# Optimization experiments

Measured on AMD Instinct MI355X. Metric: run time of the kernel, lower is better.

The kernel has to match this reference:

```python
import jax, jax.numpy as jnp
import numpy as np

EMBED = 1024
HEAD = 64
B, S = 4, 4096

def setup_inputs() -> dict:
    key = jax.random.key(0)
    k1, k2, k3, k4, k5, k6 = jax.random.split(key, 6)
    scale = 1.0 / np.sqrt(EMBED)
    return {
        "query": jax.random.normal(k1, (B, S, EMBED), dtype=jnp.float32),
        "key": jax.random.normal(k2, (B, S, EMBED), dtype=jnp.float32),
        "value": jax.random.normal(k3, (B, S, EMBED), dtype=jnp.float32),
        "wq": jax.random.normal(k4, (EMBED, HEAD), dtype=jnp.float32) * scale,
        "wk": jax.random.normal(k5, (EMBED, HEAD), dtype=jnp.float32) * scale,
        "wv": jax.random.normal(k6, (EMBED, HEAD), dtype=jnp.float32) * scale,
    }

def reference(query, key, value, wq, wk, wv):
    # projections (bias-free linears)
    q = query @ wq            # [B,S,H]
    k = key @ wk              # [B,S,H]
    v = value @ wv            # [B,S,H]
    scores = jnp.einsum('bqh,bkh->bqk', q, k) / jnp.sqrt(jnp.float32(HEAD))
    S_len = scores.shape[-1]
    causal = jnp.tril(jnp.ones((S_len, S_len), dtype=bool))
    scores = jnp.where(causal, scores, -jnp.inf)
    attn = jax.nn.softmax(scores, axis=-1)
    return attn @ v           # [B,S,H]
```

## Files before the change

kernel.cpp:

```cpp
#include <hip/hip_runtime.h>
#include <hip/hip_bf16.h>

#define EMBED 1024
#define HEAD 64
#define SEQ 4096

typedef __attribute__((ext_vector_type(8))) short short8;
typedef __attribute__((ext_vector_type(4))) float f32x4;

union S8u { short8 v; uint u[4]; ushort s[8]; };
union U4f { uint4 q; float f[4]; };

__device__ __forceinline__ ushort f2bf(float f) {
  union { float f; uint u; } x; x.f = f;
  return (ushort)((x.u + 0x7fffu + ((x.u >> 16) & 1u)) >> 16);
}

__device__ __forceinline__ ushort f2bf_n(float f) {
  union { __hip_bfloat16 h; ushort u; } cv;
  cv.h = __float2bfloat16(f);
  return cv.u;
}

__device__ __forceinline__ short8 ld16(const ushort* p) {
  uint4 q = *(const uint4*)p;
  S8u t; t.u[0] = q.x; t.u[1] = q.y; t.u[2] = q.z; t.u[3] = q.w;
  return t.v;
}

__global__ __launch_bounds__(256) void prep_w(const float* __restrict__ wq,
                                              const float* __restrict__ wk,
                                              const float* __restrict__ wv,
                                              ushort* __restrict__ wT) {
  int idx = blockIdx.x * 256 + threadIdx.x;
  if (idx >= 3 * HEAD * EMBED) return;
  int t = idx >> 16;
  int rem = idx & 0xFFFF;
  int c = rem >> 10;
  int k = rem & 1023;
  const float* w = (t == 0) ? wq : (t == 1) ? wk : wv;
  wT[idx] = f2bf_n(w[k * HEAD + c]);
}

__global__ __launch_bounds__(256, 3) void proj_kernel(
    const float* __restrict__ qsrc, const float* __restrict__ ksrc,
    const float* __restrict__ vsrc, const ushort* __restrict__ wT,
    ushort* __restrict__ qb, ushort* __restrict__ kb, ushort* __restrict__ vt) {
  __shared__ __align__(16) char smem[24576];

  const int t = blockIdx.y;
  const float* src = (t == 0) ? qsrc : (t == 1) ? ksrc : vsrc;
  const ushort* wt = wT + t * (HEAD * EMBED);
  const int tid = threadIdx.x;
  const int lane = tid & 63;
  const int wid = tid >> 6;
  const int c = lane & 15;
  const int g = lane >> 4;
  const int row0 = blockIdx.x * 64;

  const float* gA = src + (size_t)(row0 + (tid >> 4)) * EMBED + (tid & 15) * 4;
  const ushort* gB = wt + (size_t)(tid >> 3) * EMBED + (tid & 7) * 8;
  const int wA = (tid >> 4) * 256 + (((tid & 15) * 16) ^ (((tid >> 4) & 7) << 4));
  const int wB = 16384 + (tid >> 3) * 128 + (((tid & 7) * 16) ^ (((tid >> 3) & 7) << 4));

  const int rA = (wid * 16 + c) * 256;
  const int swc = (c & 7) << 4;

  f32x4 acc[4];
#pragma unroll
  for (int i = 0; i < 4; ++i) acc[i] = {0.f, 0.f, 0.f, 0.f};

  uint4 sA0 = *(const uint4*)(gA);
  uint4 sA1 = *(const uint4*)(gA + 16384);
  uint4 sA2 = *(const uint4*)(gA + 32768);
  uint4 sA3 = *(const uint4*)(gA + 49152);
  uint4 sB0 = *(const uint4*)(gB);
  uint4 sB1 = *(const uint4*)(gB + 32768);

  for (int r = 0; r < 16; ++r) {
    *(uint4*)(smem + wA)         = sA0;
    *(uint4*)(smem + wA + 4096)  = sA1;
    *(uint4*)(smem + wA + 8192)  = sA2;
    *(uint4*)(smem + wA + 12288) = sA3;
    *(uint4*)(smem + wB)         = sB0;
    *(uint4*)(smem + wB + 4096)  = sB1;
    __syncthreads();

    if (r + 1 < 16) {
      gA += 64; gB += 64;
      sA0 = *(const uint4*)(gA);
      sA1 = *(const uint4*)(gA + 16384);
      sA2 = *(const uint4*)(gA + 32768);
      sA3 = *(const uint4*)(gA + 49152);
      sB0 = *(const uint4*)(gB);
      sB1 = *(const uint4*)(gB + 32768);
    }

#pragma unroll
    for (int s = 0; s < 2; ++s) {
      U4f af0, af1;
      af0.q = *(const uint4*)(smem + rA + ((128 * s + 32 * g) ^ swc));
      af1.q = *(const uint4*)(smem + rA + ((128 * s + 32 * g + 16) ^ swc));
      S8u a;
      a.s[0] = f2bf_n(af0.f[0]); a.s[1] = f2bf_n(af0.f[1]);
      a.s[2] = f2bf_n(af0.f[2]); a.s[3] = f2bf_n(af0.f[3]);
      a.s[4] = f2bf_n(af1.f[0]); a.s[5] = f2bf_n(af1.f[1]);
      a.s[6] = f2bf_n(af1.f[2]); a.s[7] = f2bf_n(af1.f[3]);
#pragma unroll
      for (int nf = 0; nf < 4; ++nf) {
        uint4 bq = *(const uint4*)(smem + 16384 + (16 * nf + c) * 128 + ((64 * s + 16 * g) ^ swc));
        S8u b; b.u[0] = bq.x; b.u[1] = bq.y; b.u[2] = bq.z; b.u[3] = bq.w;
        acc[nf] = __builtin_amdgcn_mfma_f32_16x16x32_bf16(a.v, b.v, acc[nf], 0, 0, 0);
      }
    }
    __syncthreads();
  }

  if (t == 2) {
    ushort (*vtile)[72] = (ushort(*)[72])smem;
#pragma unroll
    for (int nf = 0; nf < 4; ++nf)
#pragma unroll
      for (int rr = 0; rr < 4; ++rr)
        vtile[nf * 16 + c][wid * 16 + 4 * g + rr] = f2bf_n(acc[nf][rr]);
    __syncthreads();
    int d = tid >> 2;
    int s0 = (tid & 3) << 4;
    int bb = row0 >> 12;
    int sbase = row0 & (SEQ - 1);
    ushort* dst = vt + ((size_t)(bb * HEAD + d) << 12) + sbase + s0;
    const uint4* srcp = (const uint4*)&vtile[d][s0];
    *(uint4*)dst = srcp[0];
    *(uint4*)(dst + 8) = srcp[1];
  } else {
    int row_base = row0 + wid * 16 + 4 * g;
    float scale = (t == 0) ? 0.18033688011112042f : 1.0f;
    ushort* dstb = (t == 0) ? qb : kb;
#pragma unroll
    for (int nf = 0; nf < 4; ++nf)
#pragma unroll
      for (int rr = 0; rr < 4; ++rr)
        dstb[(size_t)(row_base + rr) * HEAD + nf * 16 + c] = f2bf_n(acc[nf][rr] * scale);
  }
}

__global__ __launch_bounds__(512, 2) void flash_kernel(
    const ushort* __restrict__ qb, const ushort* __restrict__ kb,
    const ushort* __restrict__ vt, float* __restrict__ Opart,
    float* __restrict__ mlpart) {
  __shared__ __align__(16) char smem[16384];

  const int tid = threadIdx.x;
  const int lane = tid & 63;
  const int w = tid >> 6;
  const int c = lane & 15, g = lane >> 4;

  const int bid = blockIdx.x;
  const int band = 15 - (bid >> 4);
  const int b = (bid >> 2) & 3;
  const int j = bid & 3;
  const int ck = band + 1;
  const int kt0 = j * ck;
  const int q0w = band * 256 + w * 32;

  const int srow = tid >> 3;
  const int scol = (tid & 7) << 4;
  const int sdst = srow * 128 + (scol ^ ((srow & 7) << 4));
  const char* kgp = (const char*)(kb + (size_t)b * SEQ * HEAD) + (size_t)kt0 * 8192 + tid * 16;
  const char* vgp = (const char*)(vt + (size_t)b * HEAD * SEQ) + (size_t)srow * 8192 + kt0 * 128 + scol;

  short8 qa[2][2];
#pragma unroll
  for (int qf = 0; qf < 2; ++qf) {
    const ushort* qrow = qb + (size_t)(b * SEQ + q0w + 16 * qf + c) * HEAD + 8 * g;
    qa[qf][0] = ld16(qrow);
    qa[qf][1] = ld16(qrow + 32);
  }

  f32x4 O[4][2];
#pragma unroll
  for (int i = 0; i < 4; ++i)
#pragma unroll
    for (int qf = 0; qf < 2; ++qf) O[i][qf] = {0.f, 0.f, 0.f, 0.f};
  float m[2] = {-1e30f, -1e30f};
  float l[2] = {0.f, 0.f};

  uint4 sK = *(const uint4*)kgp;
  uint4 sV = *(const uint4*)vgp;

  for (int r = 0; r < ck; ++r) {
    *(uint4*)(smem + sdst) = sK;
    *(uint4*)(smem + 8192 + sdst) = sV;
    __syncthreads();

    if (r + 1 < ck) {
      kgp += 8192; vgp += 128;
      sK = *(const uint4*)kgp;
      sV = *(const uint4*)vgp;
    }

    const int kt = kt0 + r;
    const int k0 = kt << 6;
    if (k0 <= q0w + 31) {
      f32x4 Sf[4][2];
#pragma unroll
      for (int i = 0; i < 4; ++i)
#pragma unroll
        for (int qf = 0; qf < 2; ++qf) Sf[i][qf] = {0.f, 0.f, 0.f, 0.f};
#pragma unroll
      for (int nf = 0; nf < 4; ++nf) {
        int row = 16 * nf + c;
        int sw = (row & 7) << 4;
        uint4 kv = *(const uint4*)(smem + row * 128 + ((16 * g) ^ sw));
        S8u ka0;
        ka0.u[0] = kv.x; ka0.u[1] = kv.y; ka0.u[2] = kv.z; ka0.u[3] = kv.w;
#pragma unroll
        for (int qf = 0; qf < 2; ++qf)
          Sf[nf][qf] = __builtin_amdgcn_mfma_f32_16x16x32_bf16(ka0.v, qa[qf][0], Sf[nf][qf], 0, 0, 0);
        uint4 kv2 = *(const uint4*)(smem + row * 128 + ((64 + 16 * g) ^ sw));
        S8u ka1;
        ka1.u[0] = kv2.x; ka1.u[1] = kv2.y; ka1.u[2] = kv2.z; ka1.u[3] = kv2.w;
#pragma unroll
        for (int qf = 0; qf < 2; ++qf)
          Sf[nf][qf] = __builtin_amdgcn_mfma_f32_16x16x32_bf16(ka1.v, qa[qf][1], Sf[nf][qf], 0, 0, 0);
      }

      if (k0 + 63 > q0w) {
#pragma unroll
        for (int nf = 0; nf < 4; ++nf)
#pragma unroll
          for (int qf = 0; qf < 2; ++qf)
#pragma unroll
            for (int rr = 0; rr < 4; ++rr)
              if (k0 + nf * 16 + 4 * g + rr > q0w + 16 * qf + c) Sf[nf][qf][rr] = -1e30f;
      }

#pragma unroll
      for (int qf = 0; qf < 2; ++qf) {
        float x0 = fmaxf(fmaxf(Sf[0][qf][0], Sf[0][qf][1]), fmaxf(Sf[0][qf][2], Sf[0][qf][3]));
        float x1 = fmaxf(fmaxf(Sf[1][qf][0], Sf[1][qf][1]), fmaxf(Sf[1][qf][2], Sf[1][qf][3]));
        float x2 = fmaxf(fmaxf(Sf[2][qf][0], Sf[2][qf][1]), fmaxf(Sf[2][qf][2], Sf[2][qf][3]));
        float x3 = fmaxf(fmaxf(Sf[3][qf][0], Sf[3][qf][1]), fmaxf(Sf[3][qf][2], Sf[3][qf][3]));
        float rm = fmaxf(fmaxf(x0, x1), fmaxf(x2, x3));
        rm = fmaxf(rm, __shfl_xor(rm, 16));
        rm = fmaxf(rm, __shfl_xor(rm, 32));
        rm = fmaxf(rm, m[qf]);
        float alpha = exp2f(m[qf] - rm);
        m[qf] = rm;
#pragma unroll
        for (int nf = 0; nf < 4; ++nf)
#pragma unroll
          for (int rr = 0; rr < 4; ++rr)
            Sf[nf][qf][rr] = exp2f(Sf[nf][qf][rr] - rm);
        float s0 = (Sf[0][qf][0] + Sf[0][qf][1]) + (Sf[0][qf][2] + Sf[0][qf][3]);
        float s1 = (Sf[1][qf][0] + Sf[1][qf][1]) + (Sf[1][qf][2] + Sf[1][qf][3]);
        float s2 = (Sf[2][qf][0] + Sf[2][qf][1]) + (Sf[2][qf][2] + Sf[2][qf][3]);
        float s3 = (Sf[3][qf][0] + Sf[3][qf][1]) + (Sf[3][qf][2] + Sf[3][qf][3]);
        float rs = (s0 + s1) + (s2 + s3);
        rs += __shfl_xor(rs, 16);
        rs += __shfl_xor(rs, 32);
        l[qf] = l[qf] * alpha + rs;
#pragma unroll
        for (int nf = 0; nf < 4; ++nf)
#pragma unroll
          for (int rr = 0; rr < 4; ++rr)
            O[nf][qf][rr] *= alpha;

#pragma unroll
        for (int sl = 0; sl < 2; ++sl) {
          S8u pa;
#pragma unroll
          for (int rr = 0; rr < 4; ++rr) {
            pa.s[rr]     = f2bf(Sf[2 * sl][qf][rr]);
            pa.s[rr + 4] = f2bf(Sf[2 * sl + 1][qf][rr]);
          }
#pragma unroll
          for (int nf = 0; nf < 4; ++nf) {
            int row = 16 * nf + c;
            int sw = (row & 7) << 4;
            S8u vbf;
            uint2 lo = *(const uint2*)(smem + 8192 + row * 128 + ((64 * sl + 8 * g) ^ sw));
            uint2 hi = *(const uint2*)(smem + 8192 + row * 128 + ((64 * sl + 32 + 8 * g) ^ sw));
            vbf.u[0] = lo.x; vbf.u[1] = lo.y; vbf.u[2] = hi.x; vbf.u[3] = hi.y;
            O[nf][qf] = __builtin_amdgcn_mfma_f32_16x16x32_bf16(vbf.v, pa.v, O[nf][qf], 0, 0, 0);
          }
        }
      }
    }
    __syncthreads();
  }

  const size_t pi = (size_t)((b * 16 + band) * 4 + j);
#pragma unroll
  for (int qf = 0; qf < 2; ++qf) {
    int ql = w * 32 + 16 * qf + c;
#pragma unroll
    for (int nf = 0; nf < 4; ++nf)
      *(f32x4*)&Opart[pi * 16384 + (size_t)ql * 64 + 16 * nf + 4 * g] = O[nf][qf];
    if (g == 0) {
      mlpart[pi * 512 + ql * 2]     = m[qf];
      mlpart[pi * 512 + ql * 2 + 1] = l[qf];
    }
  }
}

__global__ __launch_bounds__(256) void merge_kernel(const float* __restrict__ Opart,
                                                    const float* __restrict__ mlpart,
                                                    float* __restrict__ out) {
  int i = blockIdx.x * 256 + threadIdx.x;
  int dq = i & 15;
  int row = i >> 4;
  int b = row >> 12;
  int qrow = row & 4095;
  int band = qrow >> 8;
  int q = qrow & 255;
  size_t pi0 = (size_t)((b * 16 + band) * 4);

  float mm[4], M = -1e30f;
#pragma unroll
  for (int jj = 0; jj < 4; ++jj) { mm[jj] = mlpart[(pi0 + jj) * 512 + q * 2]; M = fmaxf(M, mm[jj]); }
  float wgt[4], L = 0.f;
#pragma unroll
  for (int jj = 0; jj < 4; ++jj) {
    wgt[jj] = exp2f(mm[jj] - M);
    L += wgt[jj] * mlpart[(pi0 + jj) * 512 + q * 2 + 1];
  }
  f32x4 acc = {0.f, 0.f, 0.f, 0.f};
#pragma unroll
  for (int jj = 0; jj < 4; ++jj) {
    f32x4 t = *(const f32x4*)&Opart[(pi0 + jj) * 16384 + (size_t)q * 64 + 4 * dq];
#pragma unroll
    for (int rr = 0; rr < 4; ++rr) acc[rr] += wgt[jj] * t[rr];
  }
  float inv = 1.0f / L;
  f32x4 res;
#pragma unroll
  for (int rr = 0; rr < 4; ++rr) res[rr] = acc[rr] * inv;
  *(f32x4*)&out[(size_t)row * HEAD + 4 * dq] = res;
}

extern "C" void kernel_launch(void* const* d_in, const int* in_sizes, int n_in,
                              void* d_out, int out_size, void* d_ws, size_t ws_size,
                              hipStream_t stream) {
  const float* qsrc = (const float*)d_in[0];
  const float* ksrc = (const float*)d_in[1];
  const float* vsrc = (const float*)d_in[2];
  const float* wq = (const float*)d_in[3];
  const float* wk = (const float*)d_in[4];
  const float* wv = (const float*)d_in[5];
  float* out = (float*)d_out;

  char* ws = (char*)d_ws;
  ushort* wT = (ushort*)ws;
  ushort* qb = (ushort*)(ws + 393216);
  ushort* kb = (ushort*)(ws + 393216 + 2097152);
  ushort* vt = (ushort*)(ws + 393216 + 2 * 2097152);
  float* Opart = (float*)(ws + 393216 + 3 * 2097152);
  float* mlpart = (float*)(ws + 393216 + 3 * 2097152 + 16777216);

  prep_w<<<dim3(768), dim3(256), 0, stream>>>(wq, wk, wv, wT);
  proj_kernel<<<dim3(256, 3), dim3(256), 0, stream>>>(qsrc, ksrc, vsrc, wT, qb, kb, vt);
  flash_kernel<<<dim3(256), dim3(512), 0, stream>>>(qb, kb, vt, Opart, mlpart);
  merge_kernel<<<dim3(1024), dim3(256), 0, stream>>>(Opart, mlpart, out);
}
```

Measured before the change: 87.55 us.

## Use direct global-to-LDS async loads with double buffering in projection kernel

Replaces the register-staged global loads and LDS stores in the projection GEMM with global_load_lds DMA-style loads into a double-buffered shared-memory tile. Swizzling moves from the LDS write address to the global read address so each wave writes a contiguous slot. Explicit vmcnt waits let the next stage's loads overlap the current stage's MFMA work. The change doubles LDS use to 48 KB, which may reduce occupancy below the launch-bounds target of 3 blocks per CU, and it depends on the waitcnt counts being correct.

After: 88.29 us. Within noise of the previous version (+0.8%).

```diff
diff --git a/kernel.cpp b/kernel.cpp
--- a/kernel.cpp
+++ b/kernel.cpp
@@ -26,6 +26,11 @@
   uint4 q = *(const uint4*)p;
   S8u t; t.u[0] = q.x; t.u[1] = q.y; t.u[2] = q.z; t.u[3] = q.w;
   return t.v;
+}
+
+__device__ __forceinline__ void glds16(const void* g, void* l) {
+  __builtin_amdgcn_global_load_lds((const __attribute__((address_space(1))) void*)g,
+                                   (__attribute__((address_space(3))) void*)l, 16, 0, 0);
 }
 
 __global__ __launch_bounds__(256) void prep_w(const float* __restrict__ wq,
@@ -46,7 +51,7 @@
     const float* __restrict__ qsrc, const float* __restrict__ ksrc,
     const float* __restrict__ vsrc, const ushort* __restrict__ wT,
     ushort* __restrict__ qb, ushort* __restrict__ kb, ushort* __restrict__ vt) {
-  __shared__ __align__(16) char smem[24576];
+  __shared__ __align__(16) char smem[49152];
 
   const int t = blockIdx.y;
   const float* src = (t == 0) ? qsrc : (t == 1) ? ksrc : vsrc;
@@ -58,10 +63,20 @@
   const int g = lane >> 4;
   const int row0 = blockIdx.x * 64;
 
-  const float* gA = src + (size_t)(row0 + (tid >> 4)) * EMBED + (tid & 15) * 4;
-  const ushort* gB = wt + (size_t)(tid >> 3) * EMBED + (tid & 7) * 8;
-  const int wA = (tid >> 4) * 256 + (((tid & 15) * 16) ^ (((tid >> 4) & 7) << 4));
-  const int wB = 16384 + (tid >> 3) * 128 + (((tid & 7) * 16) ^ (((tid >> 3) & 7) << 4));
+  const char* gA[4];
+#pragma unroll
+  for (int mm = 0; mm < 4; ++mm) {
+    int r = mm * 16 + wid * 4 + (lane >> 4);
+    gA[mm] = (const char*)(src + (size_t)(row0 + r) * EMBED) +
+             ((((lane & 15) * 16)) ^ ((r & 7) << 4));
+  }
+  const char* gB[2];
+#pragma unroll
+  for (int m2 = 0; m2 < 2; ++m2) {
+    int r2 = m2 * 32 + wid * 8 + (lane >> 3);
+    gB[m2] = (const char*)(wt + (size_t)r2 * EMBED) +
+             ((((lane & 7) * 16)) ^ ((r2 & 7) << 4));
+  }
 
   const int rA = (wid * 16 + c) * 256;
   const int swc = (c & 7) << 4;
@@ -70,37 +85,33 @@
 #pragma unroll
   for (int i = 0; i < 4; ++i) acc[i] = {0.f, 0.f, 0.f, 0.f};
 
-  uint4 sA0 = *(const uint4*)(gA);
-  uint4 sA1 = *(const uint4*)(gA + 16384);
-  uint4 sA2 = *(const uint4*)(gA + 32768);
-  uint4 sA3 = *(const uint4*)(gA + 49152);
-  uint4 sB0 = *(const uint4*)(gB);
-  uint4 sB1 = *(const uint4*)(gB + 32768);
+#define STAGE(CUR, KOFF)                                                        \
+  do {                                                                          \
+    _Pragma("unroll") for (int mm = 0; mm < 4; ++mm)                            \
+      glds16(gA[mm] + (KOFF) * 256, smem + (CUR) * 16384 + mm * 4096 + wid * 1024); \
+    _Pragma("unroll") for (int m2 = 0; m2 < 2; ++m2)                            \
+      glds16(gB[m2] + (KOFF) * 128, smem + 32768 + (CUR) * 8192 + m2 * 4096 + wid * 1024); \
+  } while (0)
+
+  STAGE(0, 0);
 
   for (int r = 0; r < 16; ++r) {
-    *(uint4*)(smem + wA)         = sA0;
-    *(uint4*)(smem + wA + 4096)  = sA1;
-    *(uint4*)(smem + wA + 8192)  = sA2;
-    *(uint4*)(smem + wA + 12288) = sA3;
-    *(uint4*)(smem + wB)         = sB0;
-    *(uint4*)(smem + wB + 4096)  = sB1;
-    __syncthreads();
-
     if (r + 1 < 16) {
-      gA += 64; gB += 64;
-      sA0 = *(const uint4*)(gA);
-      sA1 = *(const uint4*)(gA + 16384);
-      sA2 = *(const uint4*)(gA + 32768);
-      sA3 = *(const uint4*)(gA + 49152);
-      sB0 = *(const uint4*)(gB);
-      sB1 = *(const uint4*)(gB + 32768);
-    }
-
+      STAGE((r + 1) & 1, r + 1);
+      asm volatile("s_waitcnt vmcnt(6)" ::: "memory");
+    } else {
+      asm volatile("s_waitcnt vmcnt(0)" ::: "memory");
+    }
+    __syncthreads();
+
+    const int cur = r & 1;
+    const char* bufA = smem + cur * 16384;
+    const char* bufB = smem + 32768 + cur * 8192;
 #pragma unroll
     for (int s = 0; s < 2; ++s) {
       U4f af0, af1;
-      af0.q = *(const uint4*)(smem + rA + ((128 * s + 32 * g) ^ swc));
-      af1.q = *(const uint4*)(smem + rA + ((128 * s + 32 * g + 16) ^ swc));
+      af0.q = *(const uint4*)(bufA + rA + ((128 * s + 32 * g) ^ swc));
+      af1.q = *(const uint4*)(bufA + rA + ((128 * s + 32 * g + 16) ^ swc));
       S8u a;
       a.s[0] = f2bf_n(af0.f[0]); a.s[1] = f2bf_n(af0.f[1]);
       a.s[2] = f2bf_n(af0.f[2]); a.s[3] = f2bf_n(af0.f[3]);
@@ -108,13 +119,14 @@
       a.s[6] = f2bf_n(af1.f[2]); a.s[7] = f2bf_n(af1.f[3]);
 #pragma unroll
       for (int nf = 0; nf < 4; ++nf) {
-        uint4 bq = *(const uint4*)(smem + 16384 + (16 * nf + c) * 128 + ((64 * s + 16 * g) ^ swc));
+        uint4 bq = *(const uint4*)(bufB + (16 * nf + c) * 128 + ((64 * s + 16 * g) ^ swc));
         S8u b; b.u[0] = bq.x; b.u[1] = bq.y; b.u[2] = bq.z; b.u[3] = bq.w;
         acc[nf] = __builtin_amdgcn_mfma_f32_16x16x32_bf16(a.v, b.v, acc[nf], 0, 0, 0);
       }
     }
     __syncthreads();
   }
+#undef STAGE
 
   if (t == 2) {
     ushort (*vtile)[72] = (ushort(*)[72])smem;
```
